# Performance work log

Hardware: AMD Instinct MI355X
Metric: run time of the kernel (lower is better)

The kernel has to match this reference:

```python
import jax, jax.numpy as jnp
import numpy as np

N_NODES = 100000


def _mean_agg(x, src, dst, n_nodes):
    # mean of src-node features over in-edges of each dst node (DGL copy_u + mean)
    summed = jax.ops.segment_sum(x[src], dst, num_segments=n_nodes)  # [N, F]
    deg = jax.ops.segment_sum(jnp.ones_like(src, dtype=x.dtype), dst, num_segments=n_nodes)
    return summed / jnp.maximum(deg, 1.0)[:, None]  # nodes w/o in-edges -> 0


def _sage_conv(x, src, dst, W_self, W_neigh, b):
    # DGL SAGEConv('mean'): fc_self(h) + fc_neigh(mean_neigh(h)) + bias
    h_neigh = _mean_agg(x, src, dst, x.shape[0])
    return x @ W_self + h_neigh @ W_neigh + b


def setup_inputs() -> dict:
    key = jax.random.key(0)
    ks = jax.random.split(key, 8)
    F_IN, F_H, E = 128, 128, 1600000
    s = 1.0 / np.sqrt(F_IN)
    return {
        "x": jax.random.normal(ks[0], (N_NODES, F_IN), dtype=jnp.float32),
        "src": jax.random.randint(ks[1], (E,), 0, N_NODES, dtype=jnp.int64),
        "dst": jax.random.randint(ks[2], (E,), 0, N_NODES, dtype=jnp.int64),
        "W1_self": jax.random.normal(ks[3], (F_IN, F_H), dtype=jnp.float32) * s,
        "W1_neigh": jax.random.normal(ks[4], (F_IN, F_H), dtype=jnp.float32) * s,
        "b1": jnp.zeros((F_H,), dtype=jnp.float32),
        "W2_self": jax.random.normal(ks[5], (F_H, F_H), dtype=jnp.float32) * s,
        "W2_neigh": jax.random.normal(ks[6], (F_H, F_H), dtype=jnp.float32) * s,
        "b2": jnp.zeros((F_H,), dtype=jnp.float32),
    }


def reference(x, src, dst, W1_self, W1_neigh, b1, W2_self, W2_neigh, b2):
    h = _sage_conv(x, src, dst, W1_self, W1_neigh, b1)
    # dropout in eval mode == identity
    h = jax.nn.relu(h)
    return _sage_conv(h, src, dst, W2_self, W2_neigh, b2)
```

## Files before the change

### kernel.cpp

```cpp
#include <hip/hip_runtime.h>

#define F 128
#define NN 100000
#define NBUK 782
#define NBLK 256
#define LD 136
#define N4 (NN * F / 4)
#define N4A (N4 / 2)

typedef __attribute__((ext_vector_type(8))) short short8;
typedef __attribute__((ext_vector_type(4))) float f32x4;
typedef __attribute__((ext_vector_type(4))) unsigned short us4;
typedef unsigned short ushort_t;

__device__ __forceinline__ ushort_t f2b(float f) {
    union { float f; unsigned u; } x;
    x.f = f;
    unsigned r = x.u + 0x7fffu + ((x.u >> 16) & 1u);
    return (ushort_t)(r >> 16);
}
__device__ __forceinline__ float b2f(ushort_t u) {
    union { unsigned u; float f; } x;
    x.u = ((unsigned)u) << 16;
    return x.f;
}

__global__ __launch_bounds__(256) void k1_fused(
    const int* __restrict__ dst, int* __restrict__ H, int E, int chunk,
    const float* __restrict__ Wa, const float* __restrict__ Wb,
    const float* __restrict__ Wc, const float* __restrict__ Wd,
    ushort_t* __restrict__ Oa, ushort_t* __restrict__ Ob,
    ushort_t* __restrict__ Oc, ushort_t* __restrict__ Od,
    const float* __restrict__ X, ushort_t* __restrict__ Y) {
    __shared__ union {
        int h[NBUK];
        float tile[32][33];
    } u;
    const int blk = blockIdx.x;
    if (blk < NBLK) {
        for (int i = threadIdx.x; i < NBUK; i += 256) u.h[i] = 0;
        __syncthreads();
        const int s0 = blk * chunk, s1 = min(E, s0 + chunk);
        for (int i = s0 + threadIdx.x; i < s1; i += 256)
            atomicAdd(&u.h[dst[i] >> 7], 1);
        __syncthreads();
        for (int i = threadIdx.x; i < NBUK; i += 256)
            H[blk * NBUK + i] = u.h[i];
    } else if (blk < NBLK + 64) {
        const int m = (blk - NBLK) >> 4;
        const int b = (blk - NBLK) & 15;
        const float* W = (m == 0) ? Wa : (m == 1) ? Wb : (m == 2) ? Wc : Wd;
        ushort_t* WT = (m == 0) ? Oa : (m == 1) ? Ob : (m == 2) ? Oc : Od;
        const int by = (b >> 2) * 32;
        const int bx = (b & 3) * 32;
        const int tx = threadIdx.x & 31, ty = threadIdx.x >> 5;
        for (int i = 0; i < 32; i += 8)
            u.tile[ty + i][tx] = W[(by + ty + i) * F + bx + tx];
        __syncthreads();
        for (int i = 0; i < 32; i += 8)
            WT[(bx + ty + i) * F + by + tx] = f2b(u.tile[tx][ty + i]);
    } else {
        const int i = (blk - NBLK - 64) * 256 + threadIdx.x;
        if (i < N4A) {
            float4 v = ((const float4*)X)[i];
            us4 o;
            o.x = f2b(v.x); o.y = f2b(v.y); o.z = f2b(v.z); o.w = f2b(v.w);
            ((us4*)Y)[i] = o;
        }
    }
}

__global__ __launch_bounds__(1024) void k2_fused(
    int* __restrict__ H, int* __restrict__ boffs, int E,
    const float* __restrict__ X, ushort_t* __restrict__ Y) {
    if (blockIdx.x == 0) {
        __shared__ int tot[1024];
        const int k = threadIdx.x;
        int sum = 0;
        if (k < NBUK) {
#pragma unroll 1
            for (int b = 0; b < NBLK; b += 4) {
                const int v0 = H[(b + 0) * NBUK + k];
                const int v1 = H[(b + 1) * NBUK + k];
                const int v2 = H[(b + 2) * NBUK + k];
                const int v3 = H[(b + 3) * NBUK + k];
                H[(b + 0) * NBUK + k] = sum; sum += v0;
                H[(b + 1) * NBUK + k] = sum; sum += v1;
                H[(b + 2) * NBUK + k] = sum; sum += v2;
                H[(b + 3) * NBUK + k] = sum; sum += v3;
            }
        }
        tot[k] = (k < NBUK) ? sum : 0;
        __syncthreads();
        for (int d = 1; d < 1024; d <<= 1) {
            const int u = (k >= d) ? tot[k - d] : 0;
            __syncthreads();
            tot[k] += u;
            __syncthreads();
        }
        if (k < NBUK) boffs[k] = tot[k] - sum;
        if (k == 0) boffs[NBUK] = E;
    } else {
        const int i = N4A + (blockIdx.x - 1) * 1024 + threadIdx.x;
        if (i < N4) {
            float4 v = ((const float4*)X)[i];
            us4 o;
            o.x = f2b(v.x); o.y = f2b(v.y); o.z = f2b(v.z); o.w = f2b(v.w);
            ((us4*)Y)[i] = o;
        }
    }
}

__global__ __launch_bounds__(256) void scatter2(const int* __restrict__ src,
                                                const int* __restrict__ dst,
                                                const int* __restrict__ H,
                                                const int* __restrict__ boffs,
                                                unsigned* __restrict__ pairs,
                                                int E, int chunk) {
    __shared__ int cur[NBUK];
    const int b = blockIdx.x;
    for (int i = threadIdx.x; i < NBUK; i += 256)
        cur[i] = boffs[i] + H[b * NBUK + i];
    __syncthreads();
    const int s0 = b * chunk, s1 = min(E, s0 + chunk);
    for (int i = s0 + threadIdx.x; i < s1; i += 256) {
        const int d = dst[i];
        const int p = atomicAdd(&cur[d >> 7], 1);
        pairs[p] = ((unsigned)(d & 127) << 20) | (unsigned)src[i];
    }
}

__global__ __launch_bounds__(256) void bucket_sort(const unsigned* __restrict__ pairs,
                                                   const int* __restrict__ boffs,
                                                   int* __restrict__ offs,
                                                   int* __restrict__ csr) {
    __shared__ int cnt[128], loffs[128], lcur[128];
    const int b = blockIdx.x, t = threadIdx.x;
    const int e0 = boffs[b], e1 = boffs[b + 1];
    const int node0 = b << 7;
    const int nnode = min(128, NN - node0);
    if (t < 128) cnt[t] = 0;
    __syncthreads();
    for (int i = e0 + t; i < e1; i += 256) atomicAdd(&cnt[pairs[i] >> 20], 1);
    __syncthreads();
    if (t < 128) loffs[t] = cnt[t];
    __syncthreads();
    for (int d = 1; d < 128; d <<= 1) {
        int u = (t >= d && t < 128) ? loffs[t - d] : 0;
        __syncthreads();
        if (t < 128) loffs[t] += u;
        __syncthreads();
    }
    if (t < 128) {
        const int ex = loffs[t] - cnt[t];
        lcur[t] = e0 + ex;
        if (t < nnode) offs[node0 + t] = e0 + ex;
    }
    if (b == NBUK - 1 && t == 0) offs[NN] = e1;
    __syncthreads();
    for (int i = e0 + t; i < e1; i += 256) {
        const unsigned v = pairs[i];
        const int p = atomicAdd(&lcur[v >> 20], 1);
        csr[p] = (int)(v & 0xFFFFFu);
    }
}

template <typename TOUT>
__global__ __launch_bounds__(256, 8) void sage_layer(
    const ushort_t* __restrict__ Xg,
    const int* __restrict__ offs, const int* __restrict__ csr,
    const ushort_t* __restrict__ WTs, const ushort_t* __restrict__ WTn,
    const float* __restrict__ bias,
    TOUT* __restrict__ out, int relu) {
    __shared__ __align__(16) ushort_t sX[32 * LD];
    __shared__ __align__(16) ushort_t sH[32 * LD];
    const int t = threadIdx.x;
    const int lane = t & 63;
    const int wave = t >> 6;
    const int brow0 = blockIdx.x * 32;

    {
        const ushort_t* base = Xg + (size_t)brow0 * F;
        for (int i = t; i < 32 * 16; i += 256) {
            int row = i >> 4, ch = i & 15;
            *(short8*)&sX[row * LD + ch * 8] = *(const short8*)&base[row * F + ch * 8];
        }
    }

    {
        const int slot = lane >> 4;
        const int cl = lane & 15;
        const int c8 = cl * 8;
#pragma unroll
        for (int rr = 0; rr < 2; rr++) {
            const int rloc = wave * 8 + slot * 2 + rr;
            const int row = brow0 + rloc;
            const int e0 = offs[row], e1 = offs[row + 1];
            float a0[8], a1[8], a2[8], a3[8];
#pragma unroll
            for (int j = 0; j < 8; j++) { a0[j] = a1[j] = a2[j] = a3[j] = 0.f; }
            int e = e0;
            for (; e + 3 < e1; e += 4) {
                const int s0 = csr[e], s1 = csr[e + 1], s2 = csr[e + 2], s3 = csr[e + 3];
                const short8 v0 = *(const short8*)&Xg[(size_t)s0 * F + c8];
                const short8 v1 = *(const short8*)&Xg[(size_t)s1 * F + c8];
                const short8 v2 = *(const short8*)&Xg[(size_t)s2 * F + c8];
                const short8 v3 = *(const short8*)&Xg[(size_t)s3 * F + c8];
#pragma unroll
                for (int j = 0; j < 8; j++) {
                    a0[j] += b2f((ushort_t)v0[j]);
                    a1[j] += b2f((ushort_t)v1[j]);
                    a2[j] += b2f((ushort_t)v2[j]);
                    a3[j] += b2f((ushort_t)v3[j]);
                }
            }
            for (; e < e1; e++) {
                const int s0 = csr[e];
                const short8 v0 = *(const short8*)&Xg[(size_t)s0 * F + c8];
#pragma unroll
                for (int j = 0; j < 8; j++) a0[j] += b2f((ushort_t)v0[j]);
            }
            const float inv = (e1 > e0) ? (1.0f / (float)(e1 - e0)) : 0.f;
            short8 o;
#pragma unroll
            for (int j = 0; j < 8; j++)
                o[j] = (short)f2b(((a0[j] + a1[j]) + (a2[j] + a3[j])) * inv);
            *(short8*)&sH[rloc * LD + c8] = o;
        }
    }
    __syncthreads();

    const int q = lane >> 4, nl = lane & 15;
    const int colbase = wave * 32;
    f32x4 acc00 = (f32x4)0.f, acc01 = (f32x4)0.f, acc10 = (f32x4)0.f, acc11 = (f32x4)0.f;
#pragma unroll
    for (int ks = 0; ks < 4; ks++) {
        const int ko = ks * 32 + q * 8;
        const short8 aS0 = *(const short8*)&sX[nl * LD + ko];
        const short8 aS1 = *(const short8*)&sX[(16 + nl) * LD + ko];
        const short8 aN0 = *(const short8*)&sH[nl * LD + ko];
        const short8 aN1 = *(const short8*)&sH[(16 + nl) * LD + ko];
        const size_t bo0 = (size_t)(colbase + nl) * F + ko;
        const size_t bo1 = (size_t)(colbase + 16 + nl) * F + ko;
        const short8 bS0 = *(const short8*)&WTs[bo0];
        const short8 bS1 = *(const short8*)&WTs[bo1];
        const short8 bN0 = *(const short8*)&WTn[bo0];
        const short8 bN1 = *(const short8*)&WTn[bo1];
        acc00 = __builtin_amdgcn_mfma_f32_16x16x32_bf16(aS0, bS0, acc00, 0, 0, 0);
        acc00 = __builtin_amdgcn_mfma_f32_16x16x32_bf16(aN0, bN0, acc00, 0, 0, 0);
        acc01 = __builtin_amdgcn_mfma_f32_16x16x32_bf16(aS0, bS1, acc01, 0, 0, 0);
        acc01 = __builtin_amdgcn_mfma_f32_16x16x32_bf16(aN0, bN1, acc01, 0, 0, 0);
        acc10 = __builtin_amdgcn_mfma_f32_16x16x32_bf16(aS1, bS0, acc10, 0, 0, 0);
        acc10 = __builtin_amdgcn_mfma_f32_16x16x32_bf16(aN1, bN0, acc10, 0, 0, 0);
        acc11 = __builtin_amdgcn_mfma_f32_16x16x32_bf16(aS1, bS1, acc11, 0, 0, 0);
        acc11 = __builtin_amdgcn_mfma_f32_16x16x32_bf16(aN1, bN1, acc11, 0, 0, 0);
    }

    const float b0 = bias[colbase + nl];
    const float b1 = bias[colbase + 16 + nl];
    if constexpr (sizeof(TOUT) == 2) {
        __syncthreads();
#pragma unroll
        for (int r = 0; r < 4; r++) {
            const int lr0 = q * 4 + r, lr1 = 16 + q * 4 + r;
            float v00 = acc00[r] + b0, v01 = acc01[r] + b1;
            float v10 = acc10[r] + b0, v11 = acc11[r] + b1;
            if (relu) {
                v00 = fmaxf(v00, 0.f); v01 = fmaxf(v01, 0.f);
                v10 = fmaxf(v10, 0.f); v11 = fmaxf(v11, 0.f);
            }
            sX[lr0 * LD + colbase + nl] = f2b(v00);
            sX[lr0 * LD + colbase + 16 + nl] = f2b(v01);
            sX[lr1 * LD + colbase + nl] = f2b(v10);
            sX[lr1 * LD + colbase + 16 + nl] = f2b(v11);
        }
        __syncthreads();
        TOUT* base = out + (size_t)brow0 * F;
        for (int i = t; i < 32 * 16; i += 256) {
            int row = i >> 4, ch = i & 15;
            *(short8*)&base[row * F + ch * 8] = *(const short8*)&sX[row * LD + ch * 8];
        }
    } else {
#pragma unroll
        for (int r = 0; r < 4; r++) {
            const int orow0 = brow0 + q * 4 + r;
            const int orow1 = brow0 + 16 + q * 4 + r;
            float v00 = acc00[r] + b0, v01 = acc01[r] + b1;
            float v10 = acc10[r] + b0, v11 = acc11[r] + b1;
            if (relu) {
                v00 = fmaxf(v00, 0.f); v01 = fmaxf(v01, 0.f);
                v10 = fmaxf(v10, 0.f); v11 = fmaxf(v11, 0.f);
            }
            out[(size_t)orow0 * F + colbase + nl] = v00;
            out[(size_t)orow0 * F + colbase + 16 + nl] = v01;
            out[(size_t)orow1 * F + colbase + nl] = v10;
            out[(size_t)orow1 * F + colbase + 16 + nl] = v11;
        }
    }
}

extern "C" void kernel_launch(void* const* d_in, const int* in_sizes, int n_in,
                              void* d_out, int out_size, void* d_ws, size_t ws_size,
                              hipStream_t stream) {
    const float* x = (const float*)d_in[0];
    const int* src = (const int*)d_in[1];
    const int* dst = (const int*)d_in[2];
    const float* W1s = (const float*)d_in[3];
    const float* W1n = (const float*)d_in[4];
    const float* b1 = (const float*)d_in[5];
    const float* W2s = (const float*)d_in[6];
    const float* W2n = (const float*)d_in[7];
    const float* b2 = (const float*)d_in[8];
    float* out = (float*)d_out;

    const int E = in_sizes[1];
    const int N = NN;
    const int E4 = (E + 3) & ~3;
    const int chunk = (E + NBLK - 1) / NBLK;

    unsigned* pairs = (unsigned*)d_ws;
    int* csr = (int*)(pairs + E4);
    ushort_t* h1 = (ushort_t*)(csr + E4);
    ushort_t* WT1s = h1 + (size_t)N * F;
    ushort_t* WT1n = WT1s + F * F;
    ushort_t* WT2s = WT1n + F * F;
    ushort_t* WT2n = WT2s + F * F;
    int* offs = (int*)(WT2n + F * F);
    int* H = offs + (N + 1);
    int* boffs = H + NBLK * NBUK;
    ushort_t* xb = (ushort_t*)d_out;

    const int cvtA_blocks = (N4A + 255) / 256;
    k1_fused<<<NBLK + 64 + cvtA_blocks, 256, 0, stream>>>(
        dst, H, E, chunk, W1s, W1n, W2s, W2n, WT1s, WT1n, WT2s, WT2n, x, xb);
    const int cvtB_blocks = (N4 - N4A + 1023) / 1024;
    k2_fused<<<1 + cvtB_blocks, 1024, 0, stream>>>(H, boffs, E, x, xb);
    scatter2<<<NBLK, 256, 0, stream>>>(src, dst, H, boffs, pairs, E, chunk);
    bucket_sort<<<NBUK, 256, 0, stream>>>(pairs, boffs, offs, csr);

    sage_layer<ushort_t><<<N / 32, 256, 0, stream>>>(
        xb, offs, csr, WT1s, WT1n, b1, h1, 1);
    sage_layer<float><<<N / 32, 256, 0, stream>>>(
        h1, offs, csr, WT2s, WT2n, b2, out, 0);
}
```

Baseline: 363.2 us.

## Fuse bucket sort into persistent per-bucket SAGE layer kernels

Removes the separate bucket_sort kernel and the global offs array. Each SAGE layer now runs as a persistent 1024-thread kernel that takes 128-node buckets from an atomic ticket, rebuilds per-node counts and offsets in LDS from the bucketed pairs, and then gathers, averages and runs the MFMA transform on a 128-row tile. Layer 1 also writes the CSR source lists, and layer 2 only recomputes the offsets. This saves a launch and the offs round-trip. The cost is a much larger LDS footprint per block, which likely lowers resident waves for the latency-bound gather, plus a redundant count and scan pass in layer 2 and uneven work at the end of the ticket queue.

Measured after the change: 440.7 us. 21.3% more time.

```diff
diff --git a/kernel.cpp b/kernel.cpp
--- a/kernel.cpp
+++ b/kernel.cpp
@@ -130,172 +130,190 @@
     }
 }
 
-__global__ __launch_bounds__(256) void bucket_sort(const unsigned* __restrict__ pairs,
-                                                   const int* __restrict__ boffs,
-                                                   int* __restrict__ offs,
-                                                   int* __restrict__ csr) {
-    __shared__ int cnt[128], loffs[128], lcur[128];
-    const int b = blockIdx.x, t = threadIdx.x;
-    const int e0 = boffs[b], e1 = boffs[b + 1];
-    const int node0 = b << 7;
-    const int nnode = min(128, NN - node0);
-    if (t < 128) cnt[t] = 0;
-    __syncthreads();
-    for (int i = e0 + t; i < e1; i += 256) atomicAdd(&cnt[pairs[i] >> 20], 1);
-    __syncthreads();
-    if (t < 128) loffs[t] = cnt[t];
-    __syncthreads();
-    for (int d = 1; d < 128; d <<= 1) {
-        int u = (t >= d && t < 128) ? loffs[t - d] : 0;
-        __syncthreads();
-        if (t < 128) loffs[t] += u;
-        __syncthreads();
-    }
-    if (t < 128) {
-        const int ex = loffs[t] - cnt[t];
-        lcur[t] = e0 + ex;
-        if (t < nnode) offs[node0 + t] = e0 + ex;
-    }
-    if (b == NBUK - 1 && t == 0) offs[NN] = e1;
-    __syncthreads();
-    for (int i = e0 + t; i < e1; i += 256) {
-        const unsigned v = pairs[i];
-        const int p = atomicAdd(&lcur[v >> 20], 1);
-        csr[p] = (int)(v & 0xFFFFFu);
-    }
-}
-
-template <typename TOUT>
-__global__ __launch_bounds__(256, 8) void sage_layer(
+template <typename TOUT, int DOFILL, int RELU>
+__global__ __launch_bounds__(1024, 8) void sage_bucket(
     const ushort_t* __restrict__ Xg,
-    const int* __restrict__ offs, const int* __restrict__ csr,
+    const unsigned* __restrict__ pairs,
+    const int* __restrict__ boffs,
+    int* __restrict__ csr,
     const ushort_t* __restrict__ WTs, const ushort_t* __restrict__ WTn,
     const float* __restrict__ bias,
-    TOUT* __restrict__ out, int relu) {
-    __shared__ __align__(16) ushort_t sX[32 * LD];
-    __shared__ __align__(16) ushort_t sH[32 * LD];
+    TOUT* __restrict__ out,
+    int* __restrict__ ticket) {
+    __shared__ __align__(16) ushort_t sX[128 * LD];
+    __shared__ __align__(16) ushort_t sH[128 * LD];
+    __shared__ int cnt[128], loffs[128], lcur[128];
+    __shared__ int sTile;
+
     const int t = threadIdx.x;
     const int lane = t & 63;
     const int wave = t >> 6;
-    const int brow0 = blockIdx.x * 32;
-
-    {
-        const ushort_t* base = Xg + (size_t)brow0 * F;
-        for (int i = t; i < 32 * 16; i += 256) {
-            int row = i >> 4, ch = i & 15;
-            *(short8*)&sX[row * LD + ch * 8] = *(const short8*)&base[row * F + ch * 8];
-        }
-    }
-
-    {
-        const int slot = lane >> 4;
-        const int cl = lane & 15;
-        const int c8 = cl * 8;
-#pragma unroll
-        for (int rr = 0; rr < 2; rr++) {
-            const int rloc = wave * 8 + slot * 2 + rr;
-            const int row = brow0 + rloc;
-            const int e0 = offs[row], e1 = offs[row + 1];
-            float a0[8], a1[8], a2[8], a3[8];
-#pragma unroll
-            for (int j = 0; j < 8; j++) { a0[j] = a1[j] = a2[j] = a3[j] = 0.f; }
-            int e = e0;
-            for (; e + 3 < e1; e += 4) {
-                const int s0 = csr[e], s1 = csr[e + 1], s2 = csr[e + 2], s3 = csr[e + 3];
-                const short8 v0 = *(const short8*)&Xg[(size_t)s0 * F + c8];
-                const short8 v1 = *(const short8*)&Xg[(size_t)s1 * F + c8];
-                const short8 v2 = *(const short8*)&Xg[(size_t)s2 * F + c8];
-                const short8 v3 = *(const short8*)&Xg[(size_t)s3 * F + c8];
-#pragma unroll
-                for (int j = 0; j < 8; j++) {
-                    a0[j] += b2f((ushort_t)v0[j]);
-                    a1[j] += b2f((ushort_t)v1[j]);
-                    a2[j] += b2f((ushort_t)v2[j]);
-                    a3[j] += b2f((ushort_t)v3[j]);
-                }
-            }
-            for (; e < e1; e++) {
-                const int s0 = csr[e];
-                const short8 v0 = *(const short8*)&Xg[(size_t)s0 * F + c8];
-#pragma unroll
-                for (int j = 0; j < 8; j++) a0[j] += b2f((ushort_t)v0[j]);
-            }
-            const float inv = (e1 > e0) ? (1.0f / (float)(e1 - e0)) : 0.f;
-            short8 o;
-#pragma unroll
-            for (int j = 0; j < 8; j++)
-                o[j] = (short)f2b(((a0[j] + a1[j]) + (a2[j] + a3[j])) * inv);
-            *(short8*)&sH[rloc * LD + c8] = o;
-        }
-    }
-    __syncthreads();
-
-    const int q = lane >> 4, nl = lane & 15;
-    const int colbase = wave * 32;
-    f32x4 acc00 = (f32x4)0.f, acc01 = (f32x4)0.f, acc10 = (f32x4)0.f, acc11 = (f32x4)0.f;
-#pragma unroll
-    for (int ks = 0; ks < 4; ks++) {
-        const int ko = ks * 32 + q * 8;
-        const short8 aS0 = *(const short8*)&sX[nl * LD + ko];
-        const short8 aS1 = *(const short8*)&sX[(16 + nl) * LD + ko];
-        const short8 aN0 = *(const short8*)&sH[nl * LD + ko];
-        const short8 aN1 = *(const short8*)&sH[(16 + nl) * LD + ko];
-        const size_t bo0 = (size_t)(colbase + nl) * F + ko;
-        const size_t bo1 = (size_t)(colbase + 16 + nl) * F + ko;
-        const short8 bS0 = *(const short8*)&WTs[bo0];
-        const short8 bS1 = *(const short8*)&WTs[bo1];
-        const short8 bN0 = *(const short8*)&WTn[bo0];
-        const short8 bN1 = *(const short8*)&WTn[bo1];
-        acc00 = __builtin_amdgcn_mfma_f32_16x16x32_bf16(aS0, bS0, acc00, 0, 0, 0);
-        acc00 = __builtin_amdgcn_mfma_f32_16x16x32_bf16(aN0, bN0, acc00, 0, 0, 0);
-        acc01 = __builtin_amdgcn_mfma_f32_16x16x32_bf16(aS0, bS1, acc01, 0, 0, 0);
-        acc01 = __builtin_amdgcn_mfma_f32_16x16x32_bf16(aN0, bN1, acc01, 0, 0, 0);
-        acc10 = __builtin_amdgcn_mfma_f32_16x16x32_bf16(aS1, bS0, acc10, 0, 0, 0);
-        acc10 = __builtin_amdgcn_mfma_f32_16x16x32_bf16(aN1, bN0, acc10, 0, 0, 0);
-        acc11 = __builtin_amdgcn_mfma_f32_16x16x32_bf16(aS1, bS1, acc11, 0, 0, 0);
-        acc11 = __builtin_amdgcn_mfma_f32_16x16x32_bf16(aN1, bN1, acc11, 0, 0, 0);
-    }
-
-    const float b0 = bias[colbase + nl];
-    const float b1 = bias[colbase + 16 + nl];
-    if constexpr (sizeof(TOUT) == 2) {
-        __syncthreads();
-#pragma unroll
-        for (int r = 0; r < 4; r++) {
-            const int lr0 = q * 4 + r, lr1 = 16 + q * 4 + r;
-            float v00 = acc00[r] + b0, v01 = acc01[r] + b1;
-            float v10 = acc10[r] + b0, v11 = acc11[r] + b1;
-            if (relu) {
-                v00 = fmaxf(v00, 0.f); v01 = fmaxf(v01, 0.f);
-                v10 = fmaxf(v10, 0.f); v11 = fmaxf(v11, 0.f);
-            }
-            sX[lr0 * LD + colbase + nl] = f2b(v00);
-            sX[lr0 * LD + colbase + 16 + nl] = f2b(v01);
-            sX[lr1 * LD + colbase + nl] = f2b(v10);
-            sX[lr1 * LD + colbase + 16 + nl] = f2b(v11);
-        }
-        __syncthreads();
-        TOUT* base = out + (size_t)brow0 * F;
-        for (int i = t; i < 32 * 16; i += 256) {
-            int row = i >> 4, ch = i & 15;
-            *(short8*)&base[row * F + ch * 8] = *(const short8*)&sX[row * LD + ch * 8];
-        }
-    } else {
-#pragma unroll
-        for (int r = 0; r < 4; r++) {
-            const int orow0 = brow0 + q * 4 + r;
-            const int orow1 = brow0 + 16 + q * 4 + r;
-            float v00 = acc00[r] + b0, v01 = acc01[r] + b1;
-            float v10 = acc10[r] + b0, v11 = acc11[r] + b1;
-            if (relu) {
-                v00 = fmaxf(v00, 0.f); v01 = fmaxf(v01, 0.f);
-                v10 = fmaxf(v10, 0.f); v11 = fmaxf(v11, 0.f);
-            }
-            out[(size_t)orow0 * F + colbase + nl] = v00;
-            out[(size_t)orow0 * F + colbase + 16 + nl] = v01;
-            out[(size_t)orow1 * F + colbase + nl] = v10;
-            out[(size_t)orow1 * F + colbase + 16 + nl] = v11;
-        }
+
+    for (;;) {
+        if (t == 0) sTile = atomicAdd(ticket, 1);
+        __syncthreads();
+        const int buk = sTile;
+        __syncthreads();
+        if (buk >= NBUK) break;
+
+        const int brow0 = buk << 7;
+        const int nnode = min(128, NN - brow0);
+        const int e0 = boffs[buk], e1 = boffs[buk + 1];
+
+        if (t < 128) cnt[t] = 0;
+        __syncthreads();
+        for (int i = e0 + t; i < e1; i += 1024)
+            atomicAdd(&cnt[pairs[i] >> 20], 1);
+        __syncthreads();
+        if (t < 128) loffs[t] = cnt[t];
+        __syncthreads();
+        for (int d = 1; d < 128; d <<= 1) {
+            const int u = (t < 128 && t >= d) ? loffs[t - d] : 0;
+            __syncthreads();
+            if (t < 128) loffs[t] += u;
+            __syncthreads();
+        }
+        if (t < 128) {
+            const int st = e0 + loffs[t] - cnt[t];
+            loffs[t] = st;
+            lcur[t] = st;
+        }
+        __syncthreads();
+        if (DOFILL) {
+            for (int i = e0 + t; i < e1; i += 1024) {
+                const unsigned v = pairs[i];
+                const int p = atomicAdd(&lcur[v >> 20], 1);
+                csr[p] = (int)(v & 0xFFFFFu);
+            }
+        }
+
+        {
+            const ushort_t* base = Xg + (size_t)brow0 * F;
+            for (int i = t; i < 128 * 16; i += 1024) {
+                const int row = i >> 4, ch = i & 15;
+                *(short8*)&sX[row * LD + ch * 8] = *(const short8*)&base[row * F + ch * 8];
+            }
+        }
+        __syncthreads();
+
+        {
+            const int slot = t >> 4;
+            const int c8 = (t & 15) * 8;
+#pragma unroll
+            for (int rr = 0; rr < 2; rr++) {
+                const int r = slot * 2 + rr;
+                const int es = loffs[r];
+                const int n = cnt[r];
+                const int ee = es + n;
+                float a0[8], a1[8], a2[8], a3[8];
+#pragma unroll
+                for (int j = 0; j < 8; j++) { a0[j] = a1[j] = a2[j] = a3[j] = 0.f; }
+                int e = es;
+                for (; e + 3 < ee; e += 4) {
+                    const int s0 = csr[e], s1 = csr[e + 1], s2 = csr[e + 2], s3 = csr[e + 3];
+                    const short8 v0 = *(const short8*)&Xg[(size_t)s0 * F + c8];
+                    const short8 v1 = *(const short8*)&Xg[(size_t)s1 * F + c8];
+                    const short8 v2 = *(const short8*)&Xg[(size_t)s2 * F + c8];
+                    const short8 v3 = *(const short8*)&Xg[(size_t)s3 * F + c8];
+#pragma unroll
+                    for (int j = 0; j < 8; j++) {
+                        a0[j] += b2f((ushort_t)v0[j]);
+                        a1[j] += b2f((ushort_t)v1[j]);
+                        a2[j] += b2f((ushort_t)v2[j]);
+                        a3[j] += b2f((ushort_t)v3[j]);
+                    }
+                }
+                for (; e < ee; e++) {
+                    const int s0 = csr[e];
+                    const short8 v0 = *(const short8*)&Xg[(size_t)s0 * F + c8];
+#pragma unroll
+                    for (int j = 0; j < 8; j++) a0[j] += b2f((ushort_t)v0[j]);
+                }
+                const float inv = (n > 0) ? (1.0f / (float)n) : 0.f;
+                short8 o;
+#pragma unroll
+                for (int j = 0; j < 8; j++)
+                    o[j] = (short)f2b(((a0[j] + a1[j]) + (a2[j] + a3[j])) * inv);
+                *(short8*)&sH[r * LD + c8] = o;
+            }
+        }
+        __syncthreads();
+
+        const int q = lane >> 4, nl = lane & 15;
+        const int rg = wave & 3, cg = wave >> 2;
+        const int rbase = rg * 32;
+        const int colbase = cg * 32;
+        f32x4 acc00 = (f32x4)0.f, acc01 = (f32x4)0.f, acc10 = (f32x4)0.f, acc11 = (f32x4)0.f;
+#pragma unroll
+        for (int ks = 0; ks < 4; ks++) {
+            const int ko = ks * 32 + q * 8;
+            const short8 aS0 = *(const short8*)&sX[(rbase + nl) * LD + ko];
+            const short8 aS1 = *(const short8*)&sX[(rbase + 16 + nl) * LD + ko];
+            const short8 aN0 = *(const short8*)&sH[(rbase + nl) * LD + ko];
+            const short8 aN1 = *(const short8*)&sH[(rbase + 16 + nl) * LD + ko];
+            const size_t bo0 = (size_t)(colbase + nl) * F + ko;
+            const size_t bo1 = (size_t)(colbase + 16 + nl) * F + ko;
+            const short8 bS0 = *(const short8*)&WTs[bo0];
+            const short8 bS1 = *(const short8*)&WTs[bo1];
+            const short8 bN0 = *(const short8*)&WTn[bo0];
+            const short8 bN1 = *(const short8*)&WTn[bo1];
+            acc00 = __builtin_amdgcn_mfma_f32_16x16x32_bf16(aS0, bS0, acc00, 0, 0, 0);
+            acc00 = __builtin_amdgcn_mfma_f32_16x16x32_bf16(aN0, bN0, acc00, 0, 0, 0);
+            acc01 = __builtin_amdgcn_mfma_f32_16x16x32_bf16(aS0, bS1, acc01, 0, 0, 0);
+            acc01 = __builtin_amdgcn_mfma_f32_16x16x32_bf16(aN0, bN1, acc01, 0, 0, 0);
+            acc10 = __builtin_amdgcn_mfma_f32_16x16x32_bf16(aS1, bS0, acc10, 0, 0, 0);
+            acc10 = __builtin_amdgcn_mfma_f32_16x16x32_bf16(aN1, bN0, acc10, 0, 0, 0);
+            acc11 = __builtin_amdgcn_mfma_f32_16x16x32_bf16(aS1, bS1, acc11, 0, 0, 0);
+            acc11 = __builtin_amdgcn_mfma_f32_16x16x32_bf16(aN1, bN1, acc11, 0, 0, 0);
+        }
+
+        const float b0 = bias[colbase + nl];
+        const float b1 = bias[colbase + 16 + nl];
+        if constexpr (sizeof(TOUT) == 2) {
+            __syncthreads();
+#pragma unroll
+            for (int r = 0; r < 4; r++) {
+                const int lr0 = rbase + q * 4 + r, lr1 = rbase + 16 + q * 4 + r;
+                float v00 = acc00[r] + b0, v01 = acc01[r] + b1;
+                float v10 = acc10[r] + b0, v11 = acc11[r] + b1;
+                if (RELU) {
+                    v00 = fmaxf(v00, 0.f); v01 = fmaxf(v01, 0.f);
+                    v10 = fmaxf(v10, 0.f); v11 = fmaxf(v11, 0.f);
+                }
+                sX[lr0 * LD + colbase + nl] = f2b(v00);
+                sX[lr0 * LD + colbase + 16 + nl] = f2b(v01);
+                sX[lr1 * LD + colbase + nl] = f2b(v10);
+                sX[lr1 * LD + colbase + 16 + nl] = f2b(v11);
+            }
+            __syncthreads();
+            TOUT* base = out + (size_t)brow0 * F;
+            for (int i = t; i < 128 * 16; i += 1024) {
+                const int row = i >> 4, ch = i & 15;
+                if (row < nnode)
+                    *(short8*)&base[row * F + ch * 8] = *(const short8*)&sX[row * LD + ch * 8];
+            }
+        } else {
+#pragma unroll
+            for (int r = 0; r < 4; r++) {
+                const int orow0 = brow0 + rbase + q * 4 + r;
+                const int orow1 = brow0 + rbase + 16 + q * 4 + r;
+                float v00 = acc00[r] + b0, v01 = acc01[r] + b1;
+                float v10 = acc10[r] + b0, v11 = acc11[r] + b1;
+                if (RELU) {
+                    v00 = fmaxf(v00, 0.f); v01 = fmaxf(v01, 0.f);
+                    v10 = fmaxf(v10, 0.f); v11 = fmaxf(v11, 0.f);
+                }
+                if (orow0 < NN) {
+                    out[(size_t)orow0 * F + colbase + nl] = v00;
+                    out[(size_t)orow0 * F + colbase + 16 + nl] = v01;
+                }
+                if (orow1 < NN) {
+                    out[(size_t)orow1 * F + colbase + nl] = v10;
+                    out[(size_t)orow1 * F + colbase + 16 + nl] = v11;
+                }
+            }
+        }
+        __syncthreads();
     }
 }
 
@@ -325,10 +343,12 @@
     ushort_t* WT1n = WT1s + F * F;
     ushort_t* WT2s = WT1n + F * F;
     ushort_t* WT2n = WT2s + F * F;
-    int* offs = (int*)(WT2n + F * F);
-    int* H = offs + (N + 1);
+    int* H = (int*)(WT2n + F * F);
     int* boffs = H + NBLK * NBUK;
+    int* tickets = boffs + (NBUK + 1);
     ushort_t* xb = (ushort_t*)d_out;
+
+    hipMemsetAsync(tickets, 0, 2 * sizeof(int), stream);
 
     const int cvtA_blocks = (N4A + 255) / 256;
     k1_fused<<<NBLK + 64 + cvtA_blocks, 256, 0, stream>>>(
@@ -336,10 +356,9 @@
     const int cvtB_blocks = (N4 - N4A + 1023) / 1024;
     k2_fused<<<1 + cvtB_blocks, 1024, 0, stream>>>(H, boffs, E, x, xb);
     scatter2<<<NBLK, 256, 0, stream>>>(src, dst, H, boffs, pairs, E, chunk);
-    bucket_sort<<<NBUK, 256, 0, stream>>>(pairs, boffs, offs, csr);
-
-    sage_layer<ushort_t><<<N / 32, 256, 0, stream>>>(
-        xb, offs, csr, WT1s, WT1n, b1, h1, 1);
-    sage_layer<float><<<N / 32, 256, 0, stream>>>(
-        h1, offs, csr, WT2s, WT2n, b2, out, 0);
-}
+
+    sage_bucket<ushort_t, 1, 1><<<512, 1024, 0, stream>>>(
+        xb, pairs, boffs, csr, WT1s, WT1n, b1, h1, &tickets[0]);
+    sage_bucket<float, 0, 0><<<512, 1024, 0, stream>>>(
+        h1, pairs, boffs, csr, WT2s, WT2n, b2, out, &tickets[1]);
+}
```
